# Optimization experiments

Measured on AMD Instinct MI355X. Metric: run time of the kernel, lower is better.

## Reference

```python
import jax, jax.numpy as jnp
import numpy as np

B, G, H1, H2, P, A = 8192, 20000, 512, 256, 128, 64


def setup_inputs() -> dict:
    key = jax.random.key(0)
    ks = jax.random.split(key, 9)
    s = lambda k, shape, fan: jax.random.normal(k, shape, jnp.float32) / np.sqrt(fan)
    return {
        "x": jax.random.normal(ks[0], (B, G), jnp.float32),
        "W1": s(ks[1], (H1, G), G),
        "b1": s(ks[2], (H1,), G),
        "W2": s(ks[3], (H2, H1), H1),
        "b2": s(ks[4], (H2,), H1),
        "W3": s(ks[5], (P, H2, A), H2),
        "b3": s(ks[6], (P, A), H2),
        "W4": s(ks[7], (P, A), A),
        "b4": s(ks[8], (P,), A),
    }


def reference(x, W1, b1, W2, b2, W3, b3, W4, b4):
    # shared trunk: two dense layers with ReLU (torch Linear: y = x @ W.T + b)
    h = jax.nn.relu(x @ W1.T + b1)          # [B, 512]
    h = jax.nn.relu(h @ W2.T + b2)          # [B, 256]
    # per-protein heads, batched over the protein dim P (replaces python loop)
    a = jax.nn.relu(jnp.einsum("bh,pha->bpa", h, W3) + b3)  # [B, P, A]
    out = jnp.einsum("bpa,pa->bp", a, W4) + b4               # [B, P]
    return out
```

## Files before the change

### kernel.cpp

```cpp
#include <hip/hip_runtime.h>
#include <hip/hip_bf16.h>
#include <stdint.h>

typedef unsigned short u16;
typedef __attribute__((ext_vector_type(8))) short short8;
typedef __attribute__((ext_vector_type(8))) u16   u16x8;
typedef __attribute__((ext_vector_type(4))) u16   u16x4;
typedef __attribute__((ext_vector_type(4))) float f32x4;

#define B_DIM  8192
#define G_DIM  20000
#define H1_DIM 512
#define H2_DIM 256
#define P_DIM  128
#define A_DIM  64
#define SPLITK 8
#define NKT_ALL 625

union Frag { short8 s; u16x8 u; };

__device__ __forceinline__ u16 f2b(float f) {
  union { __hip_bfloat16 b; u16 u; } c;
  c.b = __float2bfloat16(f);
  return c.u;
}

__device__ __forceinline__ void gld16(const void* g, void* l) {
  __builtin_amdgcn_global_load_lds(
      (const __attribute__((address_space(1))) void*)g,
      (__attribute__((address_space(3))) void*)l, 16, 0, 0);
}

__global__ void k_convert(const float* __restrict__ src, u16* __restrict__ dst, int n4) {
  int i = blockIdx.x * 256 + threadIdx.x;
  if (i >= n4) return;
  f32x4 v = ((const f32x4*)src)[i];
  u16x4 o;
  o[0] = f2b(v[0]); o[1] = f2b(v[1]);
  o[2] = f2b(v[2]); o[3] = f2b(v[3]);
  ((u16x4*)dst)[i] = o;
}

__global__ void k_convert_w1frag(const float* __restrict__ W1, u16* __restrict__ W1f) {
  int ot = blockIdx.x * 256 + threadIdx.x;
  if (ot >= (H1_DIM / 16) * NKT_ALL * 64) return;
  int rowblk = ot / (NKT_ALL * 64);
  int rem    = ot - rowblk * (NKT_ALL * 64);
  int kt     = rem >> 6;
  int lane   = rem & 63;
  int row = rowblk * 16 + (lane & 15);
  int col = kt * 32 + (lane >> 4) * 8;
  const float* src = W1 + (size_t)row * G_DIM + col;
  f32x4 v0 = *(const f32x4*)src;
  f32x4 v1 = *(const f32x4*)(src + 4);
  u16x8 o;
#pragma unroll
  for (int i = 0; i < 4; ++i) { o[i] = f2b(v0[i]); o[i + 4] = f2b(v1[i]); }
  ((u16x8*)W1f)[ot] = o;
}

__global__ void k_convert_w3frag(const float* __restrict__ W3, u16* __restrict__ W3f) {
  int ot = blockIdx.x * 256 + threadIdx.x;
  if (ot >= P_DIM * 4 * 8 * 64) return;
  int p    = ot >> 11;
  int rem  = ot & 2047;
  int nf   = rem >> 9;
  int kt   = (rem >> 6) & 7;
  int lane = ot & 63;
  int a  = nf * 16 + (lane & 15);
  int h0 = kt * 32 + (lane >> 4) * 8;
  u16x8 o;
#pragma unroll
  for (int j = 0; j < 8; ++j)
    o[j] = f2b(W3[((size_t)p * H2_DIM + h0 + j) * A_DIM + a]);
  ((u16x8*)W3f)[ot] = o;
}

__global__ __launch_bounds__(512, 4)
void k_gemm1(const float* __restrict__ X, const u16* __restrict__ W1f,
             float* __restrict__ partial) {
  const int ks = blockIdx.x & 7;
  const int m0 = (blockIdx.x >> 3) * 64;
  const int kt_begin = (ks == 0) ? 0 : (ks * 78 + 1);
  const int nkt = (ks == 0) ? 79 : 78;

  const int tid  = threadIdx.x;
  const int lane = tid & 63;
  const int w    = tid >> 6;
  const int c15 = lane & 15, j4 = lane >> 4;
  const int w4 = w * 4;

  __shared__ u16 lsA[2][64 * 64];

  const int aRow = tid >> 3;
  const int aG   = tid & 7;
  const int aPhysU16 = aRow * 64 + ((aG ^ (aRow & 7)) * 8);
  const float* aSrc0 = X + (size_t)(m0 + aRow) * G_DIM + aG * 8;

  f32x4 zero = {0.f, 0.f, 0.f, 0.f};
  f32x4 acc[4][4];
#pragma unroll
  for (int m = 0; m < 4; ++m)
#pragma unroll
    for (int n = 0; n < 4; ++n) acc[m][n] = zero;

  auto loadB = [&](int kt, Frag* br) {
#pragma unroll
    for (int n = 0; n < 4; ++n)
      br[n].s = *(const short8*)(W1f + ((size_t)((w4 + n) * NKT_ALL + kt) * 64 + lane) * 8);
  };
  f32x4 ar0, ar1;
  auto loadA = [&](int kt) {
    const float* src = aSrc0 + (size_t)kt * 32;
    ar0 = *(const f32x4*)src;
    ar1 = *(const f32x4*)(src + 4);
  };
  auto writeA = [&](int buf) {
    u16x8 o;
#pragma unroll
    for (int i = 0; i < 4; ++i) { o[i] = f2b(ar0[i]); o[i + 4] = f2b(ar1[i]); }
    *(u16x8*)&lsA[buf][aPhysU16] = o;
  };
  auto readAfr = [&](int buf, int half, Frag* afr) {
#pragma unroll
    for (int m = 0; m < 4; ++m) {
      int row = m * 16 + c15;
      int g = half * 4 + j4;
      int phys = g ^ (row & 7);
      afr[m].s = *(const short8*)&lsA[buf][row * 64 + phys * 8];
    }
  };

  Frag bfrE[4], bfrO[4];

  loadA(kt_begin);
  loadB(kt_begin, bfrE);
  writeA(0);
  asm volatile("s_waitcnt lgkmcnt(0)" ::: "memory");
  __builtin_amdgcn_s_barrier();
  __builtin_amdgcn_sched_barrier(0);

  const int nsuper = 39;
  for (int T = 0; T < nsuper; ++T) {
    const int buf = T & 1;
    const int kt0 = kt_begin + 2 * T;
    const int ktN = 2 * (T + 1);
    const int ktNext = kt_begin + ((ktN < nkt) ? ktN : (nkt - 1));

    loadA(ktNext);
    loadB(kt0 + 1, bfrO);

    Frag afr[4];
    readAfr(buf, 0, afr);
#pragma unroll
    for (int m = 0; m < 4; ++m)
#pragma unroll
      for (int n = 0; n < 4; ++n)
        acc[m][n] = __builtin_amdgcn_mfma_f32_16x16x32_bf16(afr[m].s, bfrE[n].s, acc[m][n], 0, 0, 0);

    loadB(ktNext, bfrE);

    readAfr(buf, 1, afr);
#pragma unroll
    for (int m = 0; m < 4; ++m)
#pragma unroll
      for (int n = 0; n < 4; ++n)
        acc[m][n] = __builtin_amdgcn_mfma_f32_16x16x32_bf16(afr[m].s, bfrO[n].s, acc[m][n], 0, 0, 0);

    writeA(buf ^ 1);
    asm volatile("s_waitcnt lgkmcnt(0)" ::: "memory");
    __builtin_amdgcn_s_barrier();
    __builtin_amdgcn_sched_barrier(0);
  }

  if (nkt == 79) {
    Frag afr[4];
    readAfr(1, 0, afr);
#pragma unroll
    for (int m = 0; m < 4; ++m)
#pragma unroll
      for (int n = 0; n < 4; ++n)
        acc[m][n] = __builtin_amdgcn_mfma_f32_16x16x32_bf16(afr[m].s, bfrE[n].s, acc[m][n], 0, 0, 0);
  }

  float* outp = partial + ((size_t)ks * B_DIM + m0) * H1_DIM;
#pragma unroll
  for (int m = 0; m < 4; ++m)
#pragma unroll
    for (int n = 0; n < 4; ++n)
#pragma unroll
      for (int r = 0; r < 4; ++r) {
        int row = m * 16 + j4 * 4 + r;
        int col = w * 64 + n * 16 + c15;
        outp[(size_t)row * H1_DIM + col] = acc[m][n][r];
      }
}

__global__ void k_reduce1(const float* __restrict__ partial, const float* __restrict__ b1,
                          u16* __restrict__ h1b) {
  const int n4 = B_DIM * H1_DIM / 4;
  int i = blockIdx.x * 256 + threadIdx.x;
  if (i >= n4) return;
  f32x4 s = ((const f32x4*)partial)[i];
#pragma unroll
  for (int k = 1; k < SPLITK; ++k) {
    f32x4 v = ((const f32x4*)partial)[(size_t)k * n4 + i];
    s[0] += v[0]; s[1] += v[1]; s[2] += v[2]; s[3] += v[3];
  }
  f32x4 bb = ((const f32x4*)b1)[i & (H1_DIM / 4 - 1)];
  u16x4 o;
#pragma unroll
  for (int j = 0; j < 4; ++j)
    o[j] = f2b(fmaxf(s[j] + bb[j], 0.f));
  ((u16x4*)h1b)[i] = o;
}

__global__ __launch_bounds__(256, 2)
void k_gemm2(const u16* __restrict__ h1b, const u16* __restrict__ W2b,
             const float* __restrict__ b2, u16* __restrict__ h2b) {
  const int m0 = blockIdx.x * 128;
  const int n0 = blockIdx.y * 64;
  const int tid  = threadIdx.x;
  const int lane = tid & 63;
  const int wid  = tid >> 6;
  const int wr = wid >> 1, wc = wid & 1;
  const int c15 = lane & 15, j4 = lane >> 4;

  __shared__ u16 lsA[2][128 * 32];
  __shared__ u16 lsB[2][64 * 32];

  f32x4 zero = {0.f, 0.f, 0.f, 0.f};
  f32x4 acc[4][2];
#pragma unroll
  for (int m = 0; m < 4; ++m) { acc[m][0] = zero; acc[m][1] = zero; }

  auto stage = [&](int buf, int kt) {
    const int k0 = kt * 32;
#pragma unroll
    for (int c = 0; c < 2; ++c) {
      int lin = c * 256 + tid;
      int row = lin >> 2, slot = lin & 3;
      int gslot = slot ^ ((row >> 1) & 3);
      gld16(h1b + (size_t)(m0 + row) * H1_DIM + k0 + gslot * 8, &lsA[buf][lin * 8]);
    }
    {
      int lin = tid;
      int row = lin >> 2, slot = lin & 3;
      int gslot = slot ^ ((row >> 1) & 3);
      gld16(W2b + (size_t)(n0 + row) * H1_DIM + k0 + gslot * 8, &lsB[buf][lin * 8]);
    }
  };

  stage(0, 0);
  __syncthreads();
  int buf = 0;
  const int nkt = H1_DIM / 32;
  for (int t = 0; t < nkt; ++t) {
    if (t + 1 < nkt) stage(buf ^ 1, t + 1);
    Frag bfr[2];
#pragma unroll
    for (int n = 0; n < 2; ++n) {
      int row = wc * 32 + n * 16 + c15;
      int slot = j4 ^ ((row >> 1) & 3);
      bfr[n].s = *(const short8*)&lsB[buf][row * 32 + slot * 8];
    }
    Frag afr[4];
#pragma unroll
    for (int m = 0; m < 4; ++m) {
      int row = wr * 64 + m * 16 + c15;
      int slot = j4 ^ ((row >> 1) & 3);
      afr[m].s = *(const short8*)&lsA[buf][row * 32 + slot * 8];
    }
#pragma unroll
    for (int m = 0; m < 4; ++m)
#pragma unroll
      for (int n = 0; n < 2; ++n)
        acc[m][n] = __builtin_amdgcn_mfma_f32_16x16x32_bf16(afr[m].s, bfr[n].s, acc[m][n], 0, 0, 0);
    __syncthreads();
    buf ^= 1;
  }

  float b2v[2];
  b2v[0] = b2[n0 + wc * 32 + c15];
  b2v[1] = b2[n0 + wc * 32 + 16 + c15];
#pragma unroll
  for (int m = 0; m < 4; ++m)
#pragma unroll
    for (int n = 0; n < 2; ++n)
#pragma unroll
      for (int r = 0; r < 4; ++r) {
        int row = m0 + wr * 64 + m * 16 + j4 * 4 + r;
        int col = n0 + wc * 32 + n * 16 + c15;
        h2b[(size_t)row * H2_DIM + col] = f2b(fmaxf(acc[m][n][r] + b2v[n], 0.f));
      }
}

__global__ __launch_bounds__(256, 2)
void k_heads(const u16* __restrict__ h2b, const u16* __restrict__ W3f,
             const float* __restrict__ b3, const float* __restrict__ W4,
             const float* __restrict__ b4, float* __restrict__ out) {
  const int pg = blockIdx.x & 15;
  const int mb = blockIdx.x >> 4;
  const int m0 = mb * 128;

  const int tid  = threadIdx.x;
  const int lane = tid & 63;
  const int w    = tid >> 6;
  const int mh = w & 1;
  const int hs = w >> 1;
  const int c15 = lane & 15, j4 = lane >> 4;

  __shared__ u16 lsA[128 * 256];

#pragma unroll
  for (int c = 0; c < 16; ++c) {
    int lin = c * 256 + tid;
    int row = lin >> 5, slot = lin & 31;
    int gslot = slot ^ (row & 7);
    gld16(h2b + (size_t)(m0 + row) * H2_DIM + gslot * 8, (u16*)lsA + lin * 8);
  }
  __syncthreads();

  f32x4 zero = {0.f, 0.f, 0.f, 0.f};

  for (int chunk = 0; chunk < 4; ++chunk) {
    const int p = pg * 8 + chunk * 2 + hs;

    f32x4 acc[4][4];
#pragma unroll
    for (int m = 0; m < 4; ++m)
#pragma unroll
      for (int n = 0; n < 4; ++n) acc[m][n] = zero;

#pragma unroll
    for (int kt = 0; kt < 8; ++kt) {
      Frag bfr[4];
#pragma unroll
      for (int nf = 0; nf < 4; ++nf)
        bfr[nf].s = *(const short8*)(W3f + (((size_t)(p * 4 + nf) * 8 + kt) * 64 + lane) * 8);
      Frag afr[4];
#pragma unroll
      for (int mf = 0; mf < 4; ++mf) {
        int row = mh * 64 + mf * 16 + c15;
        int g = kt * 4 + j4;
        int phys = g ^ (row & 7);
        afr[mf].s = *(const short8*)&lsA[row * 256 + phys * 8];
      }
#pragma unroll
      for (int mf = 0; mf < 4; ++mf)
#pragma unroll
        for (int nf = 0; nf < 4; ++nf)
          acc[mf][nf] = __builtin_amdgcn_mfma_f32_16x16x32_bf16(afr[mf].s, bfr[nf].s, acc[mf][nf], 0, 0, 0);
    }

    float w4v[4], b3v[4];
#pragma unroll
    for (int nf = 0; nf < 4; ++nf) {
      w4v[nf] = W4[p * A_DIM + nf * 16 + c15];
      b3v[nf] = b3[p * A_DIM + nf * 16 + c15];
    }
    const float b4v = b4[p];

    float s[4][4];
#pragma unroll
    for (int mf = 0; mf < 4; ++mf)
#pragma unroll
      for (int r = 0; r < 4; ++r) s[mf][r] = 0.f;
#pragma unroll
    for (int mf = 0; mf < 4; ++mf)
#pragma unroll
      for (int nf = 0; nf < 4; ++nf)
#pragma unroll
        for (int r = 0; r < 4; ++r) {
          float v = fmaxf(acc[mf][nf][r] + b3v[nf], 0.f);
          s[mf][r] += v * w4v[nf];
        }
#pragma unroll
    for (int mf = 0; mf < 4; ++mf)
#pragma unroll
      for (int r = 0; r < 4; ++r) {
        float v = s[mf][r];
        v += __shfl_xor(v, 1);
        v += __shfl_xor(v, 2);
        v += __shfl_xor(v, 4);
        v += __shfl_xor(v, 8);
        s[mf][r] = v;
      }
    if (c15 == 0) {
#pragma unroll
      for (int mf = 0; mf < 4; ++mf)
#pragma unroll
        for (int r = 0; r < 4; ++r) {
          int row = m0 + mh * 64 + mf * 16 + j4 * 4 + r;
          out[(size_t)row * P_DIM + p] = s[mf][r] + b4v;
        }
    }
  }
}

extern "C" void kernel_launch(void* const* d_in, const int* in_sizes, int n_in,
                              void* d_out, int out_size, void* d_ws, size_t ws_size,
                              hipStream_t stream) {
  const float* x  = (const float*)d_in[0];
  const float* W1 = (const float*)d_in[1];
  const float* b1 = (const float*)d_in[2];
  const float* W2 = (const float*)d_in[3];
  const float* b2 = (const float*)d_in[4];
  const float* W3 = (const float*)d_in[5];
  const float* b3 = (const float*)d_in[6];
  const float* W4 = (const float*)d_in[7];
  const float* b4 = (const float*)d_in[8];
  float* out = (float*)d_out;

  char* ws = (char*)d_ws;
  u16*   W1f  = (u16*)(ws);
  u16*   W2b  = (u16*)(ws + 20480000);
  u16*   W3f  = (u16*)(ws + 20742144);
  u16*   h1b  = (u16*)(ws + 24936448);
  u16*   h2b  = (u16*)(ws + 33325056);
  float* part = (float*)(ws + 37519360);

  k_convert_w1frag<<<dim3((1280000 + 255) / 256), dim3(256), 0, stream>>>(W1, W1f);
  k_convert<<<dim3(131072 / 4 / 256), dim3(256), 0, stream>>>(W2, W2b, 131072 / 4);
  k_convert_w3frag<<<dim3(262144 / 256), dim3(256), 0, stream>>>(W3, W3f);

  k_gemm1<<<dim3(128 * SPLITK), dim3(512), 0, stream>>>(x, W1f, part);
  k_reduce1<<<dim3(B_DIM * H1_DIM / 4 / 256), dim3(256), 0, stream>>>(part, b1, h1b);
  k_gemm2<<<dim3(64, 4), dim3(256), 0, stream>>>(h1b, W2b, b2, h2b);
  k_heads<<<dim3(1024), dim3(256), 0, stream>>>(h2b, W3f, b3, W4, b4, out);
}
```

Measured before the change: 349.6 us.

## Double GEMM1 M-tile to 128 rows and store split-K partials in bf16

Each GEMM1 block now covers 128 rows of X instead of 64, so every W1 fragment loaded from global memory feeds twice as many MFMAs and W1 traffic is halved. Launch bounds drop to 2 waves per SIMD to make room for the larger accumulator array, and the grid shrinks to 512 blocks. Split-K partial sums are now written as bf16 rather than fp32, halving partial write and reduce read traffic. The cost is lower occupancy and extra rounding error in the partials before the fp32 reduction.

```diff
diff --git a/kernel.cpp b/kernel.cpp
--- a/kernel.cpp
+++ b/kernel.cpp
@@ -23,6 +23,10 @@
   union { __hip_bfloat16 b; u16 u; } c;
   c.b = __float2bfloat16(f);
   return c.u;
+}
+__device__ __forceinline__ float b2f(u16 u) {
+  uint32_t x = ((uint32_t)u) << 16;
+  return __uint_as_float(x);
 }
 
 __device__ __forceinline__ void gld16(const void* g, void* l) {
@@ -76,11 +80,11 @@
   ((u16x8*)W3f)[ot] = o;
 }
 
-__global__ __launch_bounds__(512, 4)
+__global__ __launch_bounds__(512, 2)
 void k_gemm1(const float* __restrict__ X, const u16* __restrict__ W1f,
-             float* __restrict__ partial) {
+             u16* __restrict__ partial) {
   const int ks = blockIdx.x & 7;
-  const int m0 = (blockIdx.x >> 3) * 64;
+  const int m0 = (blockIdx.x >> 3) * 128;
   const int kt_begin = (ks == 0) ? 0 : (ks * 78 + 1);
   const int nkt = (ks == 0) ? 79 : 78;
 
@@ -90,17 +94,18 @@
   const int c15 = lane & 15, j4 = lane >> 4;
   const int w4 = w * 4;
 
-  __shared__ u16 lsA[2][64 * 64];
-
-  const int aRow = tid >> 3;
-  const int aG   = tid & 7;
-  const int aPhysU16 = aRow * 64 + ((aG ^ (aRow & 7)) * 8);
-  const float* aSrc0 = X + (size_t)(m0 + aRow) * G_DIM + aG * 8;
+  __shared__ u16 lsA[2][128 * 64];
+
+  const int aRow = tid >> 2;
+  const int aCg  = tid & 3;
+  const int aS0 = ((2 * aCg)     ^ (aRow & 7)) * 8;
+  const int aS1 = ((2 * aCg + 1) ^ (aRow & 7)) * 8;
+  const float* aSrc0 = X + (size_t)(m0 + aRow) * G_DIM + aCg * 16;
 
   f32x4 zero = {0.f, 0.f, 0.f, 0.f};
-  f32x4 acc[4][4];
-#pragma unroll
-  for (int m = 0; m < 4; ++m)
+  f32x4 acc[8][4];
+#pragma unroll
+  for (int m = 0; m < 8; ++m)
 #pragma unroll
     for (int n = 0; n < 4; ++n) acc[m][n] = zero;
 
@@ -109,21 +114,27 @@
     for (int n = 0; n < 4; ++n)
       br[n].s = *(const short8*)(W1f + ((size_t)((w4 + n) * NKT_ALL + kt) * 64 + lane) * 8);
   };
-  f32x4 ar0, ar1;
+  f32x4 ar[4];
   auto loadA = [&](int kt) {
     const float* src = aSrc0 + (size_t)kt * 32;
-    ar0 = *(const f32x4*)src;
-    ar1 = *(const f32x4*)(src + 4);
+    ar[0] = *(const f32x4*)src;
+    ar[1] = *(const f32x4*)(src + 4);
+    ar[2] = *(const f32x4*)(src + 8);
+    ar[3] = *(const f32x4*)(src + 12);
   };
   auto writeA = [&](int buf) {
-    u16x8 o;
-#pragma unroll
-    for (int i = 0; i < 4; ++i) { o[i] = f2b(ar0[i]); o[i + 4] = f2b(ar1[i]); }
-    *(u16x8*)&lsA[buf][aPhysU16] = o;
+    u16x8 o0, o1;
+#pragma unroll
+    for (int i = 0; i < 4; ++i) {
+      o0[i] = f2b(ar[0][i]); o0[i + 4] = f2b(ar[1][i]);
+      o1[i] = f2b(ar[2][i]); o1[i + 4] = f2b(ar[3][i]);
+    }
+    *(u16x8*)&lsA[buf][aRow * 64 + aS0] = o0;
+    *(u16x8*)&lsA[buf][aRow * 64 + aS1] = o1;
   };
   auto readAfr = [&](int buf, int half, Frag* afr) {
 #pragma unroll
-    for (int m = 0; m < 4; ++m) {
+    for (int m = 0; m < 8; ++m) {
       int row = m * 16 + c15;
       int g = half * 4 + j4;
       int phys = g ^ (row & 7);
@@ -150,10 +161,10 @@
     loadA(ktNext);
     loadB(kt0 + 1, bfrO);
 
-    Frag afr[4];
+    Frag afr[8];
     readAfr(buf, 0, afr);
 #pragma unroll
-    for (int m = 0; m < 4; ++m)
+    for (int m = 0; m < 8; ++m)
 #pragma unroll
       for (int n = 0; n < 4; ++n)
         acc[m][n] = __builtin_amdgcn_mfma_f32_16x16x32_bf16(afr[m].s, bfrE[n].s, acc[m][n], 0, 0, 0);
@@ -162,7 +173,7 @@
 
     readAfr(buf, 1, afr);
 #pragma unroll
-    for (int m = 0; m < 4; ++m)
+    for (int m = 0; m < 8; ++m)
 #pragma unroll
       for (int n = 0; n < 4; ++n)
         acc[m][n] = __builtin_amdgcn_mfma_f32_16x16x32_bf16(afr[m].s, bfrO[n].s, acc[m][n], 0, 0, 0);
@@ -174,45 +185,50 @@
   }
 
   if (nkt == 79) {
-    Frag afr[4];
+    Frag afr[8];
     readAfr(1, 0, afr);
 #pragma unroll
-    for (int m = 0; m < 4; ++m)
+    for (int m = 0; m < 8; ++m)
 #pragma unroll
       for (int n = 0; n < 4; ++n)
         acc[m][n] = __builtin_amdgcn_mfma_f32_16x16x32_bf16(afr[m].s, bfrE[n].s, acc[m][n], 0, 0, 0);
   }
 
-  float* outp = partial + ((size_t)ks * B_DIM + m0) * H1_DIM;
-#pragma unroll
-  for (int m = 0; m < 4; ++m)
+  u16* outp = partial + ((size_t)ks * B_DIM + m0) * H1_DIM;
+#pragma unroll
+  for (int m = 0; m < 8; ++m)
 #pragma unroll
     for (int n = 0; n < 4; ++n)
 #pragma unroll
       for (int r = 0; r < 4; ++r) {
         int row = m * 16 + j4 * 4 + r;
         int col = w * 64 + n * 16 + c15;
-        outp[(size_t)row * H1_DIM + col] = acc[m][n][r];
+        outp[(size_t)row * H1_DIM + col] = f2b(acc[m][n][r]);
       }
 }
 
-__global__ void k_reduce1(const float* __restrict__ partial, const float* __restrict__ b1,
+__global__ void k_reduce1(const u16* __restrict__ partial, const float* __restrict__ b1,
                           u16* __restrict__ h1b) {
-  const int n4 = B_DIM * H1_DIM / 4;
+  const int n8 = B_DIM * H1_DIM / 8;
   int i = blockIdx.x * 256 + threadIdx.x;
-  if (i >= n4) return;
-  f32x4 s = ((const f32x4*)partial)[i];
-#pragma unroll
-  for (int k = 1; k < SPLITK; ++k) {
-    f32x4 v = ((const f32x4*)partial)[(size_t)k * n4 + i];
-    s[0] += v[0]; s[1] += v[1]; s[2] += v[2]; s[3] += v[3];
-  }
-  f32x4 bb = ((const f32x4*)b1)[i & (H1_DIM / 4 - 1)];
-  u16x4 o;
-#pragma unroll
-  for (int j = 0; j < 4; ++j)
-    o[j] = f2b(fmaxf(s[j] + bb[j], 0.f));
-  ((u16x4*)h1b)[i] = o;
+  if (i >= n8) return;
+  float s[8] = {0.f, 0.f, 0.f, 0.f, 0.f, 0.f, 0.f, 0.f};
+#pragma unroll
+  for (int k = 0; k < SPLITK; ++k) {
+    u16x8 v = ((const u16x8*)partial)[(size_t)k * n8 + i];
+#pragma unroll
+    for (int j = 0; j < 8; ++j) s[j] += b2f(v[j]);
+  }
+  const int cb = i & (H1_DIM / 8 - 1);
+  f32x4 bb0 = ((const f32x4*)b1)[cb * 2];
+  f32x4 bb1 = ((const f32x4*)b1)[cb * 2 + 1];
+  u16x8 o;
+#pragma unroll
+  for (int j = 0; j < 4; ++j) {
+    o[j]     = f2b(fmaxf(s[j] + bb0[j], 0.f));
+    o[j + 4] = f2b(fmaxf(s[j + 4] + bb1[j], 0.f));
+  }
+  ((u16x8*)h1b)[i] = o;
 }
 
 __global__ __launch_bounds__(256, 2)
@@ -418,14 +434,14 @@
   u16*   W3f  = (u16*)(ws + 20742144);
   u16*   h1b  = (u16*)(ws + 24936448);
   u16*   h2b  = (u16*)(ws + 33325056);
-  float* part = (float*)(ws + 37519360);
+  u16*   part = (u16*)(ws + 37519360);
 
   k_convert_w1frag<<<dim3((1280000 + 255) / 256), dim3(256), 0, stream>>>(W1, W1f);
   k_convert<<<dim3(131072 / 4 / 256), dim3(256), 0, stream>>>(W2, W2b, 131072 / 4);
   k_convert_w3frag<<<dim3(262144 / 256), dim3(256), 0, stream>>>(W3, W3f);
 
-  k_gemm1<<<dim3(128 * SPLITK), dim3(512), 0, stream>>>(x, W1f, part);
-  k_reduce1<<<dim3(B_DIM * H1_DIM / 4 / 256), dim3(256), 0, stream>>>(part, b1, h1b);
+  k_gemm1<<<dim3(64 * SPLITK), dim3(512), 0, stream>>>(x, W1f, part);
+  k_reduce1<<<dim3(B_DIM * H1_DIM / 8 / 256), dim3(256), 0, stream>>>(part, b1, h1b);
   k_gemm2<<<dim3(64, 4), dim3(256), 0, stream>>>(h1b, W2b, b2, h2b);
   k_heads<<<dim3(1024), dim3(256), 0, stream>>>(h2b, W3f, b3, W4, b4, out);
 }
```

After: 320.5 us, median of 2. -8.3%, faster.
